# Performance work log

Hardware: AMD Instinct MI355X
Metric: run time of the kernel (lower is better)

Reference implementation:

```python
import jax, jax.numpy as jnp
import numpy as np

N_HEADS = 8
N_GROUPS = 32
EPS = 1e-5


def setup_inputs() -> dict:
    key = jax.random.key(0)
    ks = jax.random.split(key, 3)
    b, c, h, w = 8, 512, 32, 32
    x = jax.random.normal(ks[0], (b, c, h, w), dtype=jnp.float32)
    gamma = jnp.ones((c,), jnp.float32)
    beta = jnp.zeros((c,), jnp.float32)
    w_qkv = jax.random.normal(ks[1], (3 * c, c), jnp.float32) * (1.0 / np.sqrt(c))
    b_qkv = jnp.zeros((3 * c,), jnp.float32)
    w_proj = jax.random.normal(ks[2], (c, c), jnp.float32) * (1.0 / np.sqrt(c))
    b_proj = jnp.zeros((c,), jnp.float32)
    return {"x": x, "gamma": gamma, "beta": beta, "w_qkv": w_qkv,
            "b_qkv": b_qkv, "w_proj": w_proj, "b_proj": b_proj}


def _group_norm(x, gamma, beta):
    # x: [b, c, T]; GroupNorm over (c//G, T) per group, computed in fp32
    b, c, t = x.shape
    xg = x.reshape(b, N_GROUPS, c // N_GROUPS, t).astype(jnp.float32)
    mean = xg.mean(axis=(2, 3), keepdims=True)
    var = xg.var(axis=(2, 3), keepdims=True)
    xg = (xg - mean) * jax.lax.rsqrt(var + EPS)
    xn = xg.reshape(b, c, t).astype(x.dtype)
    return xn * gamma[None, :, None] + beta[None, :, None]


def reference(x, gamma, beta, w_qkv, b_qkv, w_proj, b_proj):
    b, c, *spatial = x.shape
    t = int(np.prod(spatial))
    xf = x.reshape(b, c, t)
    h = _group_norm(xf, gamma, beta)
    # 1x1 conv == channel matmul
    qkv = jnp.einsum('oc,bct->bot', w_qkv, h) + b_qkv[None, :, None]  # [b, 3c, t]
    ch = c // N_HEADS
    qkv = qkv.reshape(b * N_HEADS, 3 * ch, t)
    q, k, v = qkv[:, :ch], qkv[:, ch:2 * ch], qkv[:, 2 * ch:]
    scale = 1.0 / np.sqrt(np.sqrt(ch))
    weight = jnp.einsum('bct,bcs->bts', q * scale, k * scale)
    weight = jax.nn.softmax(weight.astype(jnp.float32), axis=-1).astype(weight.dtype)
    a = jnp.einsum('bts,bcs->bct', weight, v)  # [b*H, ch, t]
    a = a.reshape(b, c, t)
    h = jnp.einsum('oc,bct->bot', w_proj, a) + b_proj[None, :, None]
    return (xf + h).reshape(b, c, *spatial)
```

## Files before the change

kernel.cpp:

```cpp
#include <hip/hip_runtime.h>
#include <hip/hip_bf16.h>
#include <math.h>

#define BATCH 8
#define CDIM 512
#define TDIM 1024
#define NHD 8

typedef __attribute__((ext_vector_type(8))) _Float16 f16x8;
typedef __attribute__((ext_vector_type(4))) float floatx4;

#define QSCALE 0.18033688011112042f

static __device__ __forceinline__ unsigned short f2h(float f) {
    _Float16 h = (_Float16)f;
    return *reinterpret_cast<unsigned short*>(&h);
}
static __device__ __forceinline__ void async_load16(const unsigned short* gsrc,
                                                    unsigned short* ldst) {
    __builtin_amdgcn_global_load_lds(
        (const __attribute__((address_space(1))) void*)gsrc,
        (__attribute__((address_space(3))) void*)ldst, 16, 0, 0);
}

__global__ __launch_bounds__(256) void prep_kernel(
    const float* __restrict__ x, const float* __restrict__ gamma,
    const float* __restrict__ beta, const float* __restrict__ w_qkv,
    const float* __restrict__ w_proj, unsigned short* __restrict__ h_t,
    unsigned short* __restrict__ wq, unsigned short* __restrict__ wp) {
    int tid = threadIdx.x;
    if (blockIdx.x >= 256) {
        int i = (blockIdx.x - 256) * 256 + tid;
        const int nA = 1536 * 512 / 4;
        const float* s;
        unsigned short* d;
        int j;
        if (i < nA) { s = w_qkv; d = wq; j = i; }
        else        { s = w_proj; d = wp; j = i - nA; }
        float4 v = ((const float4*)s)[j];
        ushort4 o;
        o.x = f2h(v.x); o.y = f2h(v.y); o.z = f2h(v.z); o.w = f2h(v.w);
        ((ushort4*)d)[j] = o;
        return;
    }
    int bg = blockIdx.x;
    int b = bg >> 5, g = bg & 31;
    const float* xp = x + ((size_t)(b * CDIM + g * 16)) * TDIM;

    float s = 0.f, ss = 0.f;
    for (int r = 0; r < 16; ++r) {
        float4 v = ((const float4*)xp)[r * 256 + tid];
        s  += v.x + v.y + v.z + v.w;
        ss += v.x * v.x + v.y * v.y + v.z * v.z + v.w * v.w;
    }
    for (int off = 32; off > 0; off >>= 1) {
        s  += __shfl_down(s, off, 64);
        ss += __shfl_down(ss, off, 64);
    }
    __shared__ float rs[4], rss[4], stat[2];
    int wave = tid >> 6;
    if ((tid & 63) == 0) { rs[wave] = s; rss[wave] = ss; }
    __syncthreads();
    if (tid == 0) {
        float S  = rs[0] + rs[1] + rs[2] + rs[3];
        float SS = rss[0] + rss[1] + rss[2] + rss[3];
        float mean = S * (1.f / 16384.f);
        float var  = SS * (1.f / 16384.f) - mean * mean;
        stat[0] = mean;
        stat[1] = rsqrtf(var + 1e-5f);
    }
    __syncthreads();
    float mean = stat[0], rstd = stat[1];

    int cpair = tid & 7, trow = tid >> 3;
    int c0 = g * 16 + cpair * 2;
    float g0 = gamma[c0] * rstd,  g1 = gamma[c0 + 1] * rstd;
    float b0 = beta[c0] - mean * g0, b1 = beta[c0 + 1] - mean * g1;
    const float* x0 = x + ((size_t)(b * CDIM + c0)) * TDIM;
    const float* x1 = x0 + TDIM;
    unsigned int* hp = (unsigned int*)h_t + (size_t)b * TDIM * 256 + g * 8 + cpair;
    for (int p = 0; p < 32; ++p) {
        int t = p * 32 + trow;
        float v0 = x0[t] * g0 + b0;
        float v1 = x1[t] * g1 + b1;
        hp[(size_t)t * 256] = (unsigned)f2h(v0) | ((unsigned)f2h(v1) << 16);
    }
}

template <int BM>
__global__ __launch_bounds__(256) void mfma_gemm(
    const unsigned short* __restrict__ Wb,
    const unsigned short* __restrict__ Xt,
    const float* __restrict__ bias,
    int K, int mode,
    unsigned short* __restrict__ q_t,
    unsigned short* __restrict__ k_t,
    unsigned short* __restrict__ v,
    const float* __restrict__ resid,
    float* __restrict__ outp) {
    constexpr int AF = BM / 32;
    __shared__ __align__(16) unsigned short Bs[2 * 128 * 32];

    int tid = threadIdx.x;
    int n0 = blockIdx.x * 128, m0 = blockIdx.y * BM, bb = blockIdx.z;
    const unsigned short* Xp = Xt + (size_t)bb * TDIM * K;

    int lane = tid & 63, w = tid >> 6;
    int l15 = lane & 15, quad = lane >> 4;
    int wm = w >> 1, wn = w & 1;

    const unsigned short* aBase[AF];
#pragma unroll
    for (int mi = 0; mi < AF; ++mi)
        aBase[mi] = Wb + (size_t)(m0 + wm * (BM / 2) + mi * 16 + l15) * K + quad * 8;

    const unsigned short* bSrc[4];
    unsigned short* bDst[4];
#pragma unroll
    for (int c = 0; c < 4; ++c) {
        int slot = w * 256 + c * 64 + lane;
        int panel = slot >> 9, row = (slot >> 2) & 127, g4 = slot & 3;
        bSrc[c] = Xp + (size_t)(n0 + row) * K + panel * 32 + g4 * 8;
        bDst[c] = &Bs[(w * 256 + c * 64) * 8];
    }

    floatx4 acc[AF][4];
#pragma unroll
    for (int i = 0; i < AF; ++i)
#pragma unroll
        for (int j = 0; j < 4; ++j) acc[i][j] = (floatx4){0.f, 0.f, 0.f, 0.f};

    for (int k0 = 0; k0 < K; k0 += 64) {
        f16x8 af[AF][2];
#pragma unroll
        for (int mi = 0; mi < AF; ++mi)
#pragma unroll
            for (int kc = 0; kc < 2; ++kc)
                af[mi][kc] = *(const f16x8*)(aBase[mi] + k0 + kc * 32);
#pragma unroll
        for (int c = 0; c < 4; ++c) async_load16(bSrc[c] + k0, bDst[c]);
        __syncthreads();
#pragma unroll
        for (int kc = 0; kc < 2; ++kc) {
            f16x8 bfr[4];
#pragma unroll
            for (int ni = 0; ni < 4; ++ni)
                bfr[ni] = *(const f16x8*)&Bs[(kc * 128 + wn * 64 + ni * 16 + l15) * 32 + quad * 8];
#pragma unroll
            for (int mi = 0; mi < AF; ++mi)
#pragma unroll
                for (int ni = 0; ni < 4; ++ni)
                    acc[mi][ni] = __builtin_amdgcn_mfma_f32_16x16x32_f16(
                        af[mi][kc], bfr[ni], acc[mi][ni], 0, 0, 0);
        }
        __syncthreads();
    }

    int b8 = bb * NHD;
#pragma unroll
    for (int mi = 0; mi < AF; ++mi) {
        int mBase = m0 + wm * (BM / 2) + mi * 16 + quad * 4;
#pragma unroll
        for (int ni = 0; ni < 4; ++ni) {
            floatx4 a = acc[mi][ni];
            int n = n0 + wn * 64 + ni * 16 + l15;
            if (mode == 0) {
                int chunk = mBase >> 6;
                int hd = chunk / 3, part = chunk % 3;
                int cB = mBase & 63;
                if (part == 0) {
                    ushort4 pk;
                    pk.x = f2h((a[0] + bias[mBase + 0]) * QSCALE);
                    pk.y = f2h((a[1] + bias[mBase + 1]) * QSCALE);
                    pk.z = f2h((a[2] + bias[mBase + 2]) * QSCALE);
                    pk.w = f2h((a[3] + bias[mBase + 3]) * QSCALE);
                    *(ushort4*)&q_t[((size_t)(b8 + hd) * TDIM + n) * 64 + cB] = pk;
                } else if (part == 1) {
                    ushort4 pk;
                    pk.x = f2h(a[0] + bias[mBase + 0]);
                    pk.y = f2h(a[1] + bias[mBase + 1]);
                    pk.z = f2h(a[2] + bias[mBase + 2]);
                    pk.w = f2h(a[3] + bias[mBase + 3]);
                    *(ushort4*)&k_t[((size_t)(b8 + hd) * TDIM + n) * 64 + cB] = pk;
                } else {
#pragma unroll
                    for (int r = 0; r < 4; ++r)
                        v[((size_t)(b8 + hd) * 64 + cB + r) * TDIM + n] =
                            f2h(a[r] + bias[mBase + r]);
                }
            } else {
                size_t base = ((size_t)bb * CDIM + mBase) * TDIM + n;
#pragma unroll
                for (int r = 0; r < 4; ++r)
                    outp[base + (size_t)r * TDIM] =
                        a[r] + bias[mBase + r] + resid[base + (size_t)r * TDIM];
            }
        }
    }
}

__global__ __launch_bounds__(128, 2) void attn_kernel(
    const unsigned short* __restrict__ q_t,
    const unsigned short* __restrict__ k_t,
    const unsigned short* __restrict__ v,
    unsigned short* __restrict__ a_t) {
    __shared__ __align__(16) unsigned short Kb[2][64 * 64];
    __shared__ __align__(16) unsigned short Vb[2][64 * 64];

    int tid = threadIdx.x;
    int bh = blockIdx.x;
    int q0 = blockIdx.y * 64;
    int lane = tid & 63, w = tid >> 6;
    int l15 = lane & 15, quad = lane >> 4;
    int l7 = l15 & 7;

    const unsigned short* Qp = q_t + (size_t)bh * TDIM * 64;
    const unsigned short* Kp = k_t + (size_t)bh * TDIM * 64;
    const unsigned short* Vp = v + (size_t)bh * 64 * TDIM;

    int kofs[4], vofs[4];
    unsigned short* kdst[4];
    unsigned short* vdst[4];
#pragma unroll
    for (int c = 0; c < 4; ++c) {
        int s_ = w * 256 + c * 64 + lane;
        int m = s_ >> 3, gs = s_ & 7, g = gs ^ (m & 7);
        int mi = m >> 4, qq = (m >> 2) & 3, rr = m & 3;
        int pm = (mi & 1) * 32 + qq * 8 + (mi >> 1) * 4 + rr;
        kofs[c] = pm * 64 + g * 8;
        vofs[c] = m * TDIM + g * 8;
        kdst[c] = &Kb[0][(w * 256 + c * 64) * 8];
        vdst[c] = &Vb[0][(w * 256 + c * 64) * 8];
    }
    const int bufstep = 64 * 64;

#pragma unroll
    for (int c = 0; c < 4; ++c) {
        async_load16(Kp + kofs[c], kdst[c]);
        async_load16(Vp + vofs[c], vdst[c]);
    }

    f16x8 qf[2][2];
#pragma unroll
    for (int f = 0; f < 2; ++f)
#pragma unroll
        for (int ch = 0; ch < 2; ++ch)
            qf[f][ch] = *(const f16x8*)(Qp + (size_t)(q0 + w * 32 + f * 16 + l15) * 64 +
                                        (ch * 4 + quad) * 8);

    floatx4 o_acc[4][2];
#pragma unroll
    for (int i = 0; i < 4; ++i)
#pragma unroll
        for (int j = 0; j < 2; ++j) o_acc[i][j] = (floatx4){0.f, 0.f, 0.f, 0.f};
    float m_run[2] = {-INFINITY, -INFINITY};
    float l_run[2] = {0.f, 0.f};

    __syncthreads();

    for (int it = 0; it < 16; ++it) {
        int cur = it & 1;
        if (it < 15) {
            int s0n = (it + 1) * 64;
#pragma unroll
            for (int c = 0; c < 4; ++c) {
                async_load16(Kp + (size_t)s0n * 64 + kofs[c], kdst[c] + (cur ^ 1) * bufstep);
                async_load16(Vp + s0n + vofs[c], vdst[c] + (cur ^ 1) * bufstep);
            }
        }
        f16x8 kf[4][2];
#pragma unroll
        for (int mi = 0; mi < 4; ++mi)
#pragma unroll
            for (int ch = 0; ch < 2; ++ch)
                kf[mi][ch] = *(const f16x8*)&Kb[cur][(mi * 16 + l15) * 64 +
                                                    ((ch * 4 + quad) ^ l7) * 8];

        floatx4 sT[2][4];
#pragma unroll
        for (int f = 0; f < 2; ++f)
#pragma unroll
            for (int mi = 0; mi < 4; ++mi) {
                floatx4 z = (floatx4){0.f, 0.f, 0.f, 0.f};
                z = __builtin_amdgcn_mfma_f32_16x16x32_f16(kf[mi][0], qf[f][0], z, 0, 0, 0);
                z = __builtin_amdgcn_mfma_f32_16x16x32_f16(kf[mi][1], qf[f][1], z, 0, 0, 0);
                sT[f][mi] = z;
            }

        f16x8 vf[4][2];
#pragma unroll
        for (int ci = 0; ci < 4; ++ci)
#pragma unroll
            for (int ch = 0; ch < 2; ++ch)
                vf[ci][ch] = *(const f16x8*)&Vb[cur][(ci * 16 + l15) * 64 +
                                                    ((ch * 4 + quad) ^ l7) * 8];

        f16x8 pf[2][2];
#pragma unroll
        for (int f = 0; f < 2; ++f) {
            float mx = sT[f][0][0];
#pragma unroll
            for (int mi = 0; mi < 4; ++mi)
#pragma unroll
                for (int r = 0; r < 4; ++r) mx = fmaxf(mx, sT[f][mi][r]);
            mx = fmaxf(mx, __shfl_xor(mx, 16));
            mx = fmaxf(mx, __shfl_xor(mx, 32));
            float mn = fmaxf(m_run[f], mx);
            float alpha = __builtin_amdgcn_exp2f(m_run[f] - mn);
            float sum = 0.f;
#pragma unroll
            for (int mi = 0; mi < 4; ++mi)
#pragma unroll
                for (int r = 0; r < 4; ++r) {
                    float p = __builtin_amdgcn_exp2f(sT[f][mi][r] - mn);
                    sT[f][mi][r] = p;
                    sum += p;
                }
            sum += __shfl_xor(sum, 16);
            sum += __shfl_xor(sum, 32);
            l_run[f] = l_run[f] * alpha + sum;
            m_run[f] = mn;
#pragma unroll
            for (int ci = 0; ci < 4; ++ci) {
                o_acc[ci][f][0] *= alpha; o_acc[ci][f][1] *= alpha;
                o_acc[ci][f][2] *= alpha; o_acc[ci][f][3] *= alpha;
            }
#pragma unroll
            for (int kb = 0; kb < 2; ++kb) {
                pf[f][kb][0] = (_Float16)sT[f][kb][0];
                pf[f][kb][1] = (_Float16)sT[f][kb][1];
                pf[f][kb][2] = (_Float16)sT[f][kb][2];
                pf[f][kb][3] = (_Float16)sT[f][kb][3];
                pf[f][kb][4] = (_Float16)sT[f][kb + 2][0];
                pf[f][kb][5] = (_Float16)sT[f][kb + 2][1];
                pf[f][kb][6] = (_Float16)sT[f][kb + 2][2];
                pf[f][kb][7] = (_Float16)sT[f][kb + 2][3];
            }
        }

#pragma unroll
        for (int ci = 0; ci < 4; ++ci)
#pragma unroll
            for (int f = 0; f < 2; ++f)
#pragma unroll
                for (int kb = 0; kb < 2; ++kb)
                    o_acc[ci][f] = __builtin_amdgcn_mfma_f32_16x16x32_f16(
                        vf[ci][kb], pf[f][kb], o_acc[ci][f], 0, 0, 0);
        __syncthreads();
    }

    int b = bh >> 3, hd = bh & 7;
#pragma unroll
    for (int f = 0; f < 2; ++f) {
        float linv = 1.f / l_run[f];
        int t = q0 + w * 32 + f * 16 + l15;
        size_t rowb = ((size_t)b * TDIM + t) * CDIM + hd * 64 + quad * 4;
#pragma unroll
        for (int ci = 0; ci < 4; ++ci) {
            ushort4 pk;
            pk.x = f2h(o_acc[ci][f][0] * linv);
            pk.y = f2h(o_acc[ci][f][1] * linv);
            pk.z = f2h(o_acc[ci][f][2] * linv);
            pk.w = f2h(o_acc[ci][f][3] * linv);
            *(ushort4*)&a_t[rowb + ci * 16] = pk;
        }
    }
}

extern "C" void kernel_launch(void* const* d_in, const int* in_sizes, int n_in,
                              void* d_out, int out_size, void* d_ws, size_t ws_size,
                              hipStream_t stream) {
    (void)in_sizes; (void)n_in; (void)out_size; (void)ws_size;
    const float* x      = (const float*)d_in[0];
    const float* gamma  = (const float*)d_in[1];
    const float* beta   = (const float*)d_in[2];
    const float* w_qkv  = (const float*)d_in[3];
    const float* b_qkv  = (const float*)d_in[4];
    const float* w_proj = (const float*)d_in[5];
    const float* b_proj = (const float*)d_in[6];
    float* out = (float*)d_out;

    unsigned short* wq  = (unsigned short*)d_ws;
    unsigned short* wp  = wq + 1536 * 512;
    unsigned short* h_t = wp + 512 * 512;
    unsigned short* q_t = h_t + (size_t)BATCH * TDIM * CDIM;
    unsigned short* k_t = q_t + (size_t)64 * TDIM * 64;
    unsigned short* vv  = k_t + (size_t)64 * TDIM * 64;
    unsigned short* a_t = vv + (size_t)64 * TDIM * 64;

    prep_kernel<<<1280, 256, 0, stream>>>(x, gamma, beta, w_qkv, w_proj, h_t, wq, wp);

    mfma_gemm<128><<<dim3(8, 12, BATCH), 256, 0, stream>>>(
        wq, h_t, b_qkv, 512, 0, q_t, k_t, vv, nullptr, nullptr);

    attn_kernel<<<dim3(64, 16), 128, 0, stream>>>(q_t, k_t, vv, a_t);

    mfma_gemm<64><<<dim3(8, 8, BATCH), 256, 0, stream>>>(
        wp, a_t, b_proj, 512, 1, nullptr, nullptr, nullptr, x, out);
}
```

Measured before the change: 177.5 us.

## Stage GEMM weight tiles in swizzled LDS and transpose V output via LDS

The weight (A) operand of the QKV/proj GEMM is now loaded asynchronously into XOR-swizzled shared memory instead of being read by each lane straight from global memory. The B tile layout switches to the same 64-wide swizzled rows to avoid bank conflicts. For mode 0, the V epilogue stages each warp's tile through shared memory so it can write 16-byte coalesced rows instead of scattered 2-byte stores. This costs more LDS per block, which may reduce occupancy, and the mode-0 epilogue now only handles BM==128.

```diff
diff --git a/kernel.cpp b/kernel.cpp
--- a/kernel.cpp
+++ b/kernel.cpp
@@ -99,7 +99,8 @@
     const float* __restrict__ resid,
     float* __restrict__ outp) {
     constexpr int AF = BM / 32;
-    __shared__ __align__(16) unsigned short Bs[2 * 128 * 32];
+    __shared__ __align__(16) unsigned short As[BM * 64];
+    __shared__ __align__(16) unsigned short Bs[128 * 64];
 
     int tid = threadIdx.x;
     int n0 = blockIdx.x * 128, m0 = blockIdx.y * BM, bb = blockIdx.z;
@@ -109,18 +110,22 @@
     int l15 = lane & 15, quad = lane >> 4;
     int wm = w >> 1, wn = w & 1;
 
-    const unsigned short* aBase[AF];
-#pragma unroll
-    for (int mi = 0; mi < AF; ++mi)
-        aBase[mi] = Wb + (size_t)(m0 + wm * (BM / 2) + mi * 16 + l15) * K + quad * 8;
-
+    const unsigned short* aSrc[AF];
+    unsigned short* aDst[AF];
+#pragma unroll
+    for (int c = 0; c < AF; ++c) {
+        int slot = w * 64 * AF + c * 64 + lane;
+        int row = slot >> 3, g = (slot & 7) ^ (row & 7);
+        aSrc[c] = Wb + (size_t)(m0 + row) * K + g * 8;
+        aDst[c] = &As[(w * 64 * AF + c * 64) * 8];
+    }
     const unsigned short* bSrc[4];
     unsigned short* bDst[4];
 #pragma unroll
     for (int c = 0; c < 4; ++c) {
         int slot = w * 256 + c * 64 + lane;
-        int panel = slot >> 9, row = (slot >> 2) & 127, g4 = slot & 3;
-        bSrc[c] = Xp + (size_t)(n0 + row) * K + panel * 32 + g4 * 8;
+        int row = slot >> 3, g = (slot & 7) ^ (row & 7);
+        bSrc[c] = Xp + (size_t)(n0 + row) * K + g * 8;
         bDst[c] = &Bs[(w * 256 + c * 64) * 8];
     }
 
@@ -131,64 +136,92 @@
         for (int j = 0; j < 4; ++j) acc[i][j] = (floatx4){0.f, 0.f, 0.f, 0.f};
 
     for (int k0 = 0; k0 < K; k0 += 64) {
-        f16x8 af[AF][2];
-#pragma unroll
-        for (int mi = 0; mi < AF; ++mi)
-#pragma unroll
-            for (int kc = 0; kc < 2; ++kc)
-                af[mi][kc] = *(const f16x8*)(aBase[mi] + k0 + kc * 32);
+#pragma unroll
+        for (int c = 0; c < AF; ++c) async_load16(aSrc[c] + k0, aDst[c]);
 #pragma unroll
         for (int c = 0; c < 4; ++c) async_load16(bSrc[c] + k0, bDst[c]);
         __syncthreads();
 #pragma unroll
         for (int kc = 0; kc < 2; ++kc) {
-            f16x8 bfr[4];
-#pragma unroll
-            for (int ni = 0; ni < 4; ++ni)
-                bfr[ni] = *(const f16x8*)&Bs[(kc * 128 + wn * 64 + ni * 16 + l15) * 32 + quad * 8];
+            f16x8 af[AF], bfr[4];
+#pragma unroll
+            for (int mi = 0; mi < AF; ++mi) {
+                int row = wm * (BM / 2) + mi * 16 + l15;
+                af[mi] = *(const f16x8*)&As[row * 64 + ((kc * 4 + quad) ^ (row & 7)) * 8];
+            }
+#pragma unroll
+            for (int ni = 0; ni < 4; ++ni) {
+                int row = wn * 64 + ni * 16 + l15;
+                bfr[ni] = *(const f16x8*)&Bs[row * 64 + ((kc * 4 + quad) ^ (row & 7)) * 8];
+            }
 #pragma unroll
             for (int mi = 0; mi < AF; ++mi)
 #pragma unroll
                 for (int ni = 0; ni < 4; ++ni)
                     acc[mi][ni] = __builtin_amdgcn_mfma_f32_16x16x32_f16(
-                        af[mi][kc], bfr[ni], acc[mi][ni], 0, 0, 0);
+                        af[mi], bfr[ni], acc[mi][ni], 0, 0, 0);
         }
         __syncthreads();
     }
 
-    int b8 = bb * NHD;
-#pragma unroll
-    for (int mi = 0; mi < AF; ++mi) {
-        int mBase = m0 + wm * (BM / 2) + mi * 16 + quad * 4;
-#pragma unroll
-        for (int ni = 0; ni < 4; ++ni) {
-            floatx4 a = acc[mi][ni];
-            int n = n0 + wn * 64 + ni * 16 + l15;
-            if (mode == 0) {
-                int chunk = mBase >> 6;
-                int hd = chunk / 3, part = chunk % 3;
-                int cB = mBase & 63;
-                if (part == 0) {
-                    ushort4 pk;
-                    pk.x = f2h((a[0] + bias[mBase + 0]) * QSCALE);
-                    pk.y = f2h((a[1] + bias[mBase + 1]) * QSCALE);
-                    pk.z = f2h((a[2] + bias[mBase + 2]) * QSCALE);
-                    pk.w = f2h((a[3] + bias[mBase + 3]) * QSCALE);
-                    *(ushort4*)&q_t[((size_t)(b8 + hd) * TDIM + n) * 64 + cB] = pk;
-                } else if (part == 1) {
-                    ushort4 pk;
-                    pk.x = f2h(a[0] + bias[mBase + 0]);
-                    pk.y = f2h(a[1] + bias[mBase + 1]);
-                    pk.z = f2h(a[2] + bias[mBase + 2]);
-                    pk.w = f2h(a[3] + bias[mBase + 3]);
-                    *(ushort4*)&k_t[((size_t)(b8 + hd) * TDIM + n) * 64 + cB] = pk;
-                } else {
-#pragma unroll
-                    for (int r = 0; r < 4; ++r)
-                        v[((size_t)(b8 + hd) * 64 + cB + r) * TDIM + n] =
-                            f2h(a[r] + bias[mBase + r]);
+    if (mode == 0) {
+        if constexpr (BM == 128) {
+            int chunk = (m0 >> 6) + wm;
+            int hd = chunk / 3, part = chunk % 3;
+            int bh = bb * NHD + hd;
+            __syncthreads();
+            if (part < 2) {
+                float scale = part == 0 ? QSCALE : 1.0f;
+                unsigned short* dst = part == 0 ? q_t : k_t;
+#pragma unroll
+                for (int mi = 0; mi < 4; ++mi) {
+                    int mBase = chunk * 64 + mi * 16 + quad * 4;
+                    int cB = mBase & 63;
+#pragma unroll
+                    for (int ni = 0; ni < 4; ++ni) {
+                        floatx4 a = acc[mi][ni];
+                        int n = n0 + wn * 64 + ni * 16 + l15;
+                        ushort4 pk;
+                        pk.x = f2h((a[0] + bias[mBase + 0]) * scale);
+                        pk.y = f2h((a[1] + bias[mBase + 1]) * scale);
+                        pk.z = f2h((a[2] + bias[mBase + 2]) * scale);
+                        pk.w = f2h((a[3] + bias[mBase + 3]) * scale);
+                        *(ushort4*)&dst[((size_t)bh * TDIM + n) * 64 + cB] = pk;
+                    }
                 }
             } else {
+                unsigned short* scr = (w < 2) ? &As[w * 4096] : &Bs[(w - 2) * 4096];
+#pragma unroll
+                for (int mi = 0; mi < 4; ++mi)
+#pragma unroll
+                    for (int ni = 0; ni < 4; ++ni) {
+                        floatx4 a = acc[mi][ni];
+#pragma unroll
+                        for (int r = 0; r < 4; ++r) {
+                            int c = mi * 16 + quad * 4 + r;
+                            int j = ni * 16 + l15;
+                            int seg = j >> 3;
+                            scr[c * 64 + ((seg ^ (c & 7)) * 8) + (j & 7)] =
+                                f2h(a[r] + bias[chunk * 64 + c]);
+                        }
+                    }
+                int rr = lane >> 3, seg = lane & 7;
+#pragma unroll
+                for (int it = 0; it < 8; ++it) {
+                    int c = it * 8 + rr;
+                    uint4 val = *(const uint4*)&scr[c * 64 + ((seg ^ (c & 7)) * 8)];
+                    *(uint4*)&v[((size_t)bh * 64 + c) * TDIM + n0 + wn * 64 + seg * 8] = val;
+                }
+            }
+        }
+    } else {
+#pragma unroll
+        for (int mi = 0; mi < AF; ++mi) {
+            int mBase = m0 + wm * (BM / 2) + mi * 16 + quad * 4;
+#pragma unroll
+            for (int ni = 0; ni < 4; ++ni) {
+                floatx4 a = acc[mi][ni];
+                int n = n0 + wn * 64 + ni * 16 + l15;
                 size_t base = ((size_t)bb * CDIM + mBase) * TDIM + n;
 #pragma unroll
                 for (int r = 0; r < 4; ++r)
```

Result: faster. 156.2 us (-12.0%).
